# Optimization experiments

Hardware: AMD Instinct MI355X
Metric: run time of the kernel (lower is better)

## Reference

```python
import jax, jax.numpy as jnp
import numpy as np

TOPK = 2
ALPHA = 32.0
EPS = 1e-20


def setup_inputs() -> dict:
    key = jax.random.key(0)
    ks = jax.random.split(key, 6)
    E, D, R, Q, V = 16, 2048, 16, 2048, 512
    B, S = 2, 2048
    return {
        "hidden_states": jax.random.normal(ks[0], (B, S, D), jnp.float32),
        "router_weight": jax.random.normal(ks[1], (E, D), jnp.float32) * 0.02,
        "q_lora_a": jax.random.normal(ks[2], (E, D, R), jnp.float32) * 0.02,
        "q_lora_b": jax.random.normal(ks[3], (E, R, Q), jnp.float32) * 0.02,
        "v_lora_a": jax.random.normal(ks[4], (E, D, R), jnp.float32) * 0.02,
        "v_lora_b": jax.random.normal(ks[5], (E, R, V), jnp.float32) * 0.02,
    }


def reference(hidden_states, router_weight, q_lora_a, q_lora_b, v_lora_a, v_lora_b):
    E, D, R = q_lora_a.shape
    Qo = q_lora_b.shape[-1]
    Vo = v_lora_b.shape[-1]
    scale = ALPHA / float(R)
    orig_shape = hidden_states.shape[:-1]
    h = hidden_states.reshape(-1, D)  # [n, D]
    n = h.shape[0]

    # router: top-k softmax probs, renormalized over the k selected experts
    logits = jnp.einsum('nd,ed->ne', h, router_weight)
    probs = jax.nn.softmax(logits, axis=-1)
    scores, idx = jax.lax.top_k(probs, TOPK)          # [n, k]
    scores = scores / (scores.sum(-1, keepdims=True) + EPS)

    # per-token expert combine weights c[n, e] = scale * sum_k score_k * 1[idx_k == e]
    c = jnp.zeros((n, E), h.dtype).at[jnp.arange(n)[:, None], idx].add(scores * scale)

    # dense per-expert low-rank projections; weighting by c makes non-selected
    # experts contribute zero -> identical math to gather + einsum + weighted sum.
    q_low = jnp.einsum('nd,edr->ner', h, q_lora_a) * c[..., None]  # [n, E, R]
    v_low = jnp.einsum('nd,edr->ner', h, v_lora_a) * c[..., None]
    q_delta = jnp.einsum('ner,erq->nq', q_low, q_lora_b)
    v_delta = jnp.einsum('ner,erv->nv', v_low, v_lora_b)

    return (q_delta.reshape(*orig_shape, Qo), v_delta.reshape(*orig_shape, Vo))
```

## Files before the change

### kernel.cpp

```cpp
#include <hip/hip_runtime.h>
#include <math.h>

#define DD 2048
#define EE 16
#define RR 16
#define QO 2048
#define VO 512
#define DSPLIT 4
#define DRANGE (DD / DSPLIT)
#define DC 64
#define HSTR (DC + 4)
#define ASTR 20
#define RDC 256
#define TB 32
#define ACHUNKS 32
#define T2 32
#define CGQ (QO / 256)
#define CGV (VO / 256)

struct Route { int i0, i1; float w0, w1; };

__global__ void zero_cnt(int* __restrict__ cnt) {
    if (threadIdx.x < EE) cnt[threadIdx.x] = 0;
}

__global__ __launch_bounds__(256) void router_kernel(
    const float* __restrict__ h, const float* __restrict__ rw,
    Route* __restrict__ route, unsigned short* __restrict__ bucket,
    int* __restrict__ cnt, int n)
{
    __shared__ float  hs[8 * RDC];
    __shared__ double slogd[8 * EE];

    int t0 = blockIdx.x * 8;
    int e  = threadIdx.x >> 4;
    int l  = threadIdx.x & 15;

    double acc[8];
#pragma unroll
    for (int t = 0; t < 8; ++t) acc[t] = 0.0;

    for (int d0 = 0; d0 < DD; d0 += RDC) {
        __syncthreads();
        for (int i = threadIdx.x; i < 8 * (RDC / 4); i += 256) {
            int t = i >> 6, dq = (i & 63) * 4;
            float4 v = make_float4(0.f, 0.f, 0.f, 0.f);
            if (t0 + t < n)
                v = *(const float4*)&h[(size_t)(t0 + t) * DD + d0 + dq];
            *(float4*)&hs[t * RDC + dq] = v;
        }
        __syncthreads();
        const float* rwe = rw + e * DD + d0;
#pragma unroll
        for (int g = 0; g < RDC / 64; ++g) {
            int d = g * 64 + l * 4;
            float4 r4 = *(const float4*)&rwe[d];
            double rx = r4.x, ry = r4.y, rz = r4.z, rw4 = r4.w;
#pragma unroll
            for (int t = 0; t < 8; ++t) {
                float4 hv = *(const float4*)&hs[t * RDC + d];
                acc[t] += (double)hv.x * rx + (double)hv.y * ry
                        + (double)hv.z * rz + (double)hv.w * rw4;
            }
        }
    }
#pragma unroll
    for (int t = 0; t < 8; ++t) {
#pragma unroll
        for (int off = 8; off; off >>= 1)
            acc[t] += __shfl_down(acc[t], off, 16);
    }
    if (l == 0) {
#pragma unroll
        for (int t = 0; t < 8; ++t) slogd[t * EE + e] = acc[t];
    }
    __syncthreads();

    if (threadIdx.x < 8) {
        int t = threadIdx.x, tok = t0 + t;
        if (tok < n) {
            double lg[EE];
#pragma unroll
            for (int i = 0; i < EE; ++i) lg[i] = slogd[t * EE + i];
            int i0 = 0;
            for (int i = 1; i < EE; ++i) if (lg[i] > lg[i0]) i0 = i;
            int i1 = -1;
            for (int i = 0; i < EE; ++i)
                if (i != i0 && (i1 < 0 || lg[i] > lg[i1])) i1 = i;
            double ed = exp(lg[i1] - lg[i0]);
            double w0 = 2.0 / (1.0 + ed);
            Route rt;
            rt.i0 = i0; rt.i1 = i1;
            rt.w0 = (float)w0;
            rt.w1 = (float)(2.0 - w0);
            route[tok] = rt;
            int p0 = atomicAdd(&cnt[i0], 1);
            bucket[(size_t)i0 * n + p0] = (unsigned short)(tok * 2);
            int p1 = atomicAdd(&cnt[i1], 1);
            bucket[(size_t)i1 * n + p1] = (unsigned short)(tok * 2 + 1);
        }
    }
}

__global__ __launch_bounds__(256) void a_kernel(
    const float* __restrict__ h, const Route* __restrict__ route,
    const unsigned short* __restrict__ bucket, const int* __restrict__ cnt,
    const float* __restrict__ qa, const float* __restrict__ va,
    float* __restrict__ low, int n)
{
    int e  = blockIdx.x;
    int ds = blockIdx.z;
    int cnt_e = cnt[e];

    __shared__ int   sel_tok[TB];
    __shared__ int   sel_k[TB];
    __shared__ float sel_w[TB];
    __align__(16) __shared__ float aq_s[DC * ASTR];
    __align__(16) __shared__ float av_s[DC * ASTR];
    __align__(16) __shared__ float hs[TB * HSTR];

    const float* qa_e = qa + (size_t)e * DD * RR;
    const float* va_e = va + (size_t)e * DD * RR;

    int s    = threadIdx.x & 15;
    int tile = threadIdx.x >> 4;
    int tp   = tile >> 2;
    int rp   = tile & 3;

    for (int c0 = blockIdx.y * TB; c0 < cnt_e; c0 += gridDim.y * TB) {
        int mb = min(TB, cnt_e - c0);
        if (threadIdx.x < TB && threadIdx.x < mb) {
            int slot = bucket[(size_t)e * n + c0 + threadIdx.x];
            int tok = slot >> 1, k = slot & 1;
            Route rt = route[tok];
            sel_tok[threadIdx.x] = tok;
            sel_k[threadIdx.x]   = k;
            sel_w[threadIdx.x]   = k ? rt.w1 : rt.w0;
        }
        float accq[8][4], accv[8][4];
#pragma unroll
        for (int ti = 0; ti < 8; ++ti)
#pragma unroll
            for (int ri = 0; ri < 4; ++ri) { accq[ti][ri] = 0.f; accv[ti][ri] = 0.f; }

        for (int d0 = ds * DRANGE; d0 < (ds + 1) * DRANGE; d0 += DC) {
            __syncthreads();
            {
                int i = threadIdx.x;
                int d = i >> 2, rf = (i & 3) * 4;
                *(float4*)&aq_s[d * ASTR + rf] = *(const float4*)&qa_e[(size_t)(d0 + d) * RR + rf];
                *(float4*)&av_s[d * ASTR + rf] = *(const float4*)&va_e[(size_t)(d0 + d) * RR + rf];
            }
            for (int i = threadIdx.x; i < TB * (DC / 4); i += 256) {
                int j = i >> 4, dq = (i & 15) * 4;
                float4 v = make_float4(0.f, 0.f, 0.f, 0.f);
                if (j < mb)
                    v = *(const float4*)&h[(size_t)sel_tok[j] * DD + d0 + dq];
                *(float4*)&hs[j * HSTR + dq] = v;
            }
            __syncthreads();
#pragma unroll
            for (int dd = 0; dd < DC / 16; ++dd) {
                int d = (dd << 4) + s;
                float hv[8];
#pragma unroll
                for (int ti = 0; ti < 8; ++ti)
                    hv[ti] = hs[(tp * 8 + ti) * HSTR + d];
                float4 aqv = *(const float4*)&aq_s[d * ASTR + rp * 4];
                float4 avv = *(const float4*)&av_s[d * ASTR + rp * 4];
                const float* aqp = &aqv.x;
                const float* avp = &avv.x;
#pragma unroll
                for (int ti = 0; ti < 8; ++ti)
#pragma unroll
                    for (int ri = 0; ri < 4; ++ri) {
                        accq[ti][ri] = fmaf(hv[ti], aqp[ri], accq[ti][ri]);
                        accv[ti][ri] = fmaf(hv[ti], avp[ri], accv[ti][ri]);
                    }
            }
        }
#pragma unroll
        for (int ti = 0; ti < 8; ++ti)
#pragma unroll
            for (int ri = 0; ri < 4; ++ri) {
#pragma unroll
                for (int off = 8; off; off >>= 1) {
                    accq[ti][ri] += __shfl_down(accq[ti][ri], off, 16);
                    accv[ti][ri] += __shfl_down(accv[ti][ri], off, 16);
                }
            }
        if (s == 0) {
#pragma unroll
            for (int ti = 0; ti < 8; ++ti) {
                int t = tp * 8 + ti;
                if (t < mb) {
                    int   tok = sel_tok[t];
                    int   k   = sel_k[t];
                    float w   = sel_w[t];
                    size_t base = ((size_t)(tok * 2 + k) * DSPLIT + ds) * 32;
                    float4 q4 = make_float4(accq[ti][0] * w, accq[ti][1] * w,
                                            accq[ti][2] * w, accq[ti][3] * w);
                    float4 v4 = make_float4(accv[ti][0] * w, accv[ti][1] * w,
                                            accv[ti][2] * w, accv[ti][3] * w);
                    *(float4*)&low[base + rp * 4]      = q4;
                    *(float4*)&low[base + 16 + rp * 4] = v4;
                }
            }
        }
        __syncthreads();
    }
}

__global__ __launch_bounds__(256) void b_kernel(
    const Route* __restrict__ route, const float* __restrict__ low,
    const float* __restrict__ qb, const float* __restrict__ vb,
    float* __restrict__ outq, float* __restrict__ outv, int n)
{
    int t0 = blockIdx.x * T2;
    int cg = blockIdx.y;
    int tid = threadIdx.x;

    __shared__ float part[T2 * 2 * 256];
    __shared__ float ls[T2 * 2 * RR];
    __shared__ int   elist[EE * T2];
    __shared__ int   ecnt[EE];
    __shared__ Route rts[T2];

    if (tid < EE) ecnt[tid] = 0;
    if (tid < T2) {
        int tok = t0 + tid;
        if (tok < n) rts[tid] = route[tok];
        else { rts[tid].i0 = -1; rts[tid].i1 = -1; rts[tid].w0 = 0.f; rts[tid].w1 = 0.f; }
    }
    __syncthreads();
    if (tid < T2 * 2) {
        int j = tid >> 1, k = tid & 1;
        int e = k ? rts[j].i1 : rts[j].i0;
        if (e >= 0) {
            int p = atomicAdd(&ecnt[e], 1);
            elist[e * T2 + p] = j * 2 + k;
        }
    }
    int side = (cg >= CGQ) ? 1 : 0;
    {
        int slot = tid >> 2, r4 = (tid & 3) * 4;
        int j = slot >> 1, k = slot & 1;
        int tok = t0 + j;
        float4 v = make_float4(0.f, 0.f, 0.f, 0.f);
        if (tok < n) {
            const float* lp = low + (size_t)(tok * 2 + k) * (DSPLIT * 32) + side * 16 + r4;
            float4 p0 = *(const float4*)(lp);
            float4 p1 = *(const float4*)(lp + 32);
            float4 p2 = *(const float4*)(lp + 64);
            float4 p3 = *(const float4*)(lp + 96);
            v.x = p0.x + p1.x + p2.x + p3.x;
            v.y = p0.y + p1.y + p2.y + p3.y;
            v.z = p0.z + p1.z + p2.z + p3.z;
            v.w = p0.w + p1.w + p2.w + p3.w;
        }
        *(float4*)&ls[slot * RR + r4] = v;
    }
    __syncthreads();

    const float* bp; float* outp; int W, colbase;
    if (cg < CGQ) { bp = qb; outp = outq; W = QO; colbase = cg * 256; }
    else          { bp = vb; outp = outv; W = VO; colbase = (cg - CGQ) * 256; }
    int col = colbase + tid;

    float bcA[RR], bcB[RR];
    {
        const float* be = bp + col;
#pragma unroll
        for (int r = 0; r < RR; ++r) bcA[r] = be[(size_t)r * W];
    }

#define PROC_E(EI, BC)                                                      \
    {                                                                       \
        int c = ecnt[EI];                                                   \
        for (int ii = 0; ii < c; ++ii) {                                    \
            int sk = elist[(EI) * T2 + ii];                                 \
            const float* lp = &ls[sk * RR];                                 \
            float4 l0 = *(const float4*)(lp);                               \
            float4 l1 = *(const float4*)(lp + 4);                           \
            float4 l2 = *(const float4*)(lp + 8);                           \
            float4 l3 = *(const float4*)(lp + 12);                          \
            float v = 0.f;                                                  \
            v = fmaf(l0.x, BC[0],  v); v = fmaf(l0.y, BC[1],  v);           \
            v = fmaf(l0.z, BC[2],  v); v = fmaf(l0.w, BC[3],  v);           \
            v = fmaf(l1.x, BC[4],  v); v = fmaf(l1.y, BC[5],  v);           \
            v = fmaf(l1.z, BC[6],  v); v = fmaf(l1.w, BC[7],  v);           \
            v = fmaf(l2.x, BC[8],  v); v = fmaf(l2.y, BC[9],  v);           \
            v = fmaf(l2.z, BC[10], v); v = fmaf(l2.w, BC[11], v);           \
            v = fmaf(l3.x, BC[12], v); v = fmaf(l3.y, BC[13], v);           \
            v = fmaf(l3.z, BC[14], v); v = fmaf(l3.w, BC[15], v);           \
            part[sk * 256 + tid] = v;                                       \
        }                                                                   \
    }

    for (int e = 0; e < EE; e += 2) {
        {
            const float* bn = bp + (size_t)(e + 1) * RR * W + col;
#pragma unroll
            for (int r = 0; r < RR; ++r) bcB[r] = bn[(size_t)r * W];
        }
        PROC_E(e, bcA);
        if (e + 2 < EE) {
            const float* bn = bp + (size_t)(e + 2) * RR * W + col;
#pragma unroll
            for (int r = 0; r < RR; ++r) bcA[r] = bn[(size_t)r * W];
        }
        PROC_E(e + 1, bcB);
    }
#undef PROC_E

#pragma unroll
    for (int j = 0; j < T2; ++j) {
        int tok = t0 + j;
        if (tok < n)
            outp[(size_t)tok * W + col] =
                part[(j * 2) * 256 + tid] + part[(j * 2 + 1) * 256 + tid];
    }
}

extern "C" void kernel_launch(void* const* d_in, const int* in_sizes, int n_in,
                              void* d_out, int out_size, void* d_ws, size_t ws_size,
                              hipStream_t stream) {
    const float* h  = (const float*)d_in[0];
    const float* rw = (const float*)d_in[1];
    const float* qa = (const float*)d_in[2];
    const float* qb = (const float*)d_in[3];
    const float* va = (const float*)d_in[4];
    const float* vb = (const float*)d_in[5];

    int n = in_sizes[0] / DD;
    float* out  = (float*)d_out;
    float* outq = out;
    float* outv = out + (size_t)n * QO;

    char* ws = (char*)d_ws;
    Route* route = (Route*)ws;
    size_t off = ((size_t)n * sizeof(Route) + 255) & ~(size_t)255;
    int* cnt = (int*)(ws + off);
    off = (off + EE * sizeof(int) + 255) & ~(size_t)255;
    unsigned short* bucket = (unsigned short*)(ws + off);
    off = (off + (size_t)EE * n * sizeof(unsigned short) + 255) & ~(size_t)255;
    float* low = (float*)(ws + off);

    zero_cnt<<<1, 64, 0, stream>>>(cnt);

    router_kernel<<<(n + 7) / 8, 256, 0, stream>>>(h, rw, route, bucket, cnt, n);

    dim3 g2(EE, ACHUNKS, DSPLIT);
    a_kernel<<<g2, 256, 0, stream>>>(h, route, bucket, cnt, qa, va, low, n);

    dim3 g3((n + T2 - 1) / T2, CGQ + CGV);
    b_kernel<<<g3, 256, 0, stream>>>(route, low, qb, vb, outq, outv, n);
}
```

Measured before the change: 243.0 us.

## Split router over D across blocks, add finalize kernel, shrink b_kernel shared memory

```diff
diff --git a/kernel.cpp b/kernel.cpp
--- a/kernel.cpp
+++ b/kernel.cpp
@@ -12,8 +12,9 @@
 #define HSTR (DC + 4)
 #define ASTR 20
 #define RDC 256
+#define DSPL 8
 #define TB 32
-#define ACHUNKS 32
+#define ACHUNKS 16
 #define T2 32
 #define CGQ (QO / 256)
 #define CGV (VO / 256)
@@ -24,44 +25,42 @@
     if (threadIdx.x < EE) cnt[threadIdx.x] = 0;
 }
 
-__global__ __launch_bounds__(256) void router_kernel(
+__global__ __launch_bounds__(256) void logits_kernel(
     const float* __restrict__ h, const float* __restrict__ rw,
-    Route* __restrict__ route, unsigned short* __restrict__ bucket,
-    int* __restrict__ cnt, int n)
+    double* __restrict__ lgp, int n)
 {
-    __shared__ float  hs[8 * RDC];
-    __shared__ double slogd[8 * EE];
+    __shared__ float hs[8 * RDC];
 
     int t0 = blockIdx.x * 8;
+    int ds = blockIdx.y;
+    int d0 = ds * RDC;
     int e  = threadIdx.x >> 4;
     int l  = threadIdx.x & 15;
 
+    for (int i = threadIdx.x; i < 8 * (RDC / 4); i += 256) {
+        int t = i >> 6, dq = (i & 63) * 4;
+        float4 v = make_float4(0.f, 0.f, 0.f, 0.f);
+        if (t0 + t < n)
+            v = *(const float4*)&h[(size_t)(t0 + t) * DD + d0 + dq];
+        *(float4*)&hs[t * RDC + dq] = v;
+    }
+    __syncthreads();
+
     double acc[8];
 #pragma unroll
     for (int t = 0; t < 8; ++t) acc[t] = 0.0;
 
-    for (int d0 = 0; d0 < DD; d0 += RDC) {
-        __syncthreads();
-        for (int i = threadIdx.x; i < 8 * (RDC / 4); i += 256) {
-            int t = i >> 6, dq = (i & 63) * 4;
-            float4 v = make_float4(0.f, 0.f, 0.f, 0.f);
-            if (t0 + t < n)
-                v = *(const float4*)&h[(size_t)(t0 + t) * DD + d0 + dq];
-            *(float4*)&hs[t * RDC + dq] = v;
-        }
-        __syncthreads();
-        const float* rwe = rw + e * DD + d0;
-#pragma unroll
-        for (int g = 0; g < RDC / 64; ++g) {
-            int d = g * 64 + l * 4;
-            float4 r4 = *(const float4*)&rwe[d];
-            double rx = r4.x, ry = r4.y, rz = r4.z, rw4 = r4.w;
-#pragma unroll
-            for (int t = 0; t < 8; ++t) {
-                float4 hv = *(const float4*)&hs[t * RDC + d];
-                acc[t] += (double)hv.x * rx + (double)hv.y * ry
-                        + (double)hv.z * rz + (double)hv.w * rw4;
-            }
+    const float* rwe = rw + e * DD + d0;
+#pragma unroll
+    for (int g = 0; g < RDC / 64; ++g) {
+        int d = g * 64 + l * 4;
+        float4 r4 = *(const float4*)&rwe[d];
+        double rx = r4.x, ry = r4.y, rz = r4.z, rw4 = r4.w;
+#pragma unroll
+        for (int t = 0; t < 8; ++t) {
+            float4 hv = *(const float4*)&hs[t * RDC + d];
+            acc[t] += (double)hv.x * rx + (double)hv.y * ry
+                    + (double)hv.z * rz + (double)hv.w * rw4;
         }
     }
 #pragma unroll
@@ -72,34 +71,46 @@
     }
     if (l == 0) {
 #pragma unroll
-        for (int t = 0; t < 8; ++t) slogd[t * EE + e] = acc[t];
-    }
-    __syncthreads();
-
-    if (threadIdx.x < 8) {
-        int t = threadIdx.x, tok = t0 + t;
-        if (tok < n) {
-            double lg[EE];
-#pragma unroll
-            for (int i = 0; i < EE; ++i) lg[i] = slogd[t * EE + i];
-            int i0 = 0;
-            for (int i = 1; i < EE; ++i) if (lg[i] > lg[i0]) i0 = i;
-            int i1 = -1;
-            for (int i = 0; i < EE; ++i)
-                if (i != i0 && (i1 < 0 || lg[i] > lg[i1])) i1 = i;
-            double ed = exp(lg[i1] - lg[i0]);
-            double w0 = 2.0 / (1.0 + ed);
-            Route rt;
-            rt.i0 = i0; rt.i1 = i1;
-            rt.w0 = (float)w0;
-            rt.w1 = (float)(2.0 - w0);
-            route[tok] = rt;
-            int p0 = atomicAdd(&cnt[i0], 1);
-            bucket[(size_t)i0 * n + p0] = (unsigned short)(tok * 2);
-            int p1 = atomicAdd(&cnt[i1], 1);
-            bucket[(size_t)i1 * n + p1] = (unsigned short)(tok * 2 + 1);
-        }
-    }
+        for (int t = 0; t < 8; ++t) {
+            int tok = t0 + t;
+            if (tok < n)
+                lgp[((size_t)tok * DSPL + ds) * EE + e] = acc[t];
+        }
+    }
+}
+
+__global__ __launch_bounds__(256) void finalize_kernel(
+    const double* __restrict__ lgp, Route* __restrict__ route,
+    unsigned short* __restrict__ bucket, int* __restrict__ cnt, int n)
+{
+    int tok = blockIdx.x * 256 + threadIdx.x;
+    if (tok >= n) return;
+
+    double lg[EE];
+#pragma unroll
+    for (int e = 0; e < EE; ++e) lg[e] = 0.0;
+    const double* p = lgp + (size_t)tok * (DSPL * EE);
+#pragma unroll
+    for (int ds = 0; ds < DSPL; ++ds)
+#pragma unroll
+        for (int e = 0; e < EE; ++e) lg[e] += p[ds * EE + e];
+
+    int i0 = 0;
+    for (int i = 1; i < EE; ++i) if (lg[i] > lg[i0]) i0 = i;
+    int i1 = -1;
+    for (int i = 0; i < EE; ++i)
+        if (i != i0 && (i1 < 0 || lg[i] > lg[i1])) i1 = i;
+    double ed = exp(lg[i1] - lg[i0]);
+    double w0 = 2.0 / (1.0 + ed);
+    Route rt;
+    rt.i0 = i0; rt.i1 = i1;
+    rt.w0 = (float)w0;
+    rt.w1 = (float)(2.0 - w0);
+    route[tok] = rt;
+    int p0 = atomicAdd(&cnt[i0], 1);
+    bucket[(size_t)i0 * n + p0] = (unsigned short)(tok * 2);
+    int p1 = atomicAdd(&cnt[i1], 1);
+    bucket[(size_t)i1 * n + p1] = (unsigned short)(tok * 2 + 1);
 }
 
 __global__ __launch_bounds__(256) void a_kernel(
@@ -220,7 +231,7 @@
     int cg = blockIdx.y;
     int tid = threadIdx.x;
 
-    __shared__ float part[T2 * 2 * 256];
+    __shared__ float acc_s[T2 * 256];
     __shared__ float ls[T2 * 2 * RR];
     __shared__ int   elist[EE * T2];
     __shared__ int   ecnt[EE];
@@ -260,6 +271,8 @@
         }
         *(float4*)&ls[slot * RR + r4] = v;
     }
+#pragma unroll
+    for (int j = 0; j < T2; ++j) acc_s[j * 256 + tid] = 0.f;
     __syncthreads();
 
     const float* bp; float* outp; int W, colbase;
@@ -293,7 +306,7 @@
             v = fmaf(l2.z, BC[10], v); v = fmaf(l2.w, BC[11], v);           \
             v = fmaf(l3.x, BC[12], v); v = fmaf(l3.y, BC[13], v);           \
             v = fmaf(l3.z, BC[14], v); v = fmaf(l3.w, BC[15], v);           \
-            part[sk * 256 + tid] = v;                                       \
+            acc_s[(sk >> 1) * 256 + tid] += v;   \
         }                                                                   \
     }
 
@@ -316,9 +329,7 @@
 #pragma unroll
     for (int j = 0; j < T2; ++j) {
         int tok = t0 + j;
-        if (tok < n)
-            outp[(size_t)tok * W + col] =
-                part[(j * 2) * 256 + tid] + part[(j * 2 + 1) * 256 + tid];
+        if (tok < n) outp[(size_t)tok * W + col] = acc_s[j * 256 + tid];
     }
 }
 
@@ -345,10 +356,14 @@
     unsigned short* bucket = (unsigned short*)(ws + off);
     off = (off + (size_t)EE * n * sizeof(unsigned short) + 255) & ~(size_t)255;
     float* low = (float*)(ws + off);
+    double* lgp = (double*)low;
 
     zero_cnt<<<1, 64, 0, stream>>>(cnt);
 
-    router_kernel<<<(n + 7) / 8, 256, 0, stream>>>(h, rw, route, bucket, cnt, n);
+    dim3 g1((n + 7) / 8, DSPL);
+    logits_kernel<<<g1, 256, 0, stream>>>(h, rw, lgp, n);
+
+    finalize_kernel<<<(n + 255) / 256, 256, 0, stream>>>(lgp, route, bucket, cnt, n);
 
     dim3 g2(EE, ACHUNKS, DSPLIT);
     a_kernel<<<g2, 256, 0, stream>>>(h, route, bucket, cnt, qa, va, low, n);
```

New measurement: 240.6 us. About the same (-1.0%).
